# Optimization experiments

Hardware: AMD Instinct MI355X
Metric: run time of the kernel (lower is better)

## Reference

```python
import jax, jax.numpy as jnp
import numpy as np

Q, L = 512, 4096


def setup_inputs() -> dict:
    key = jax.random.key(0)
    ks = jax.random.split(key, 12)
    def rn(k, shape, s=0.05):
        return jax.random.normal(k, shape, jnp.float32) * s
    return {
        "reactions": jax.random.normal(ks[0], (1, Q, 256), jnp.float32),
        "protein":   jax.random.normal(ks[1], (1, L, 1024), jnp.float32),
        # conv1d(1024->256, k=1) == pointwise linear
        "Wc":  rn(ks[2], (256, 1024)), "bc":  jnp.zeros((256,), jnp.float32),
        "W1":  rn(ks[3], (64, 256)),   "b1":  jnp.zeros((64,), jnp.float32),
        "W2":  rn(ks[4], (64, 256)),   "b2":  jnp.zeros((64,), jnp.float32),
        "Wa":  rn(ks[5], (64, 64)),    "ba":  jnp.zeros((64,), jnp.float32),
        "Wpa": rn(ks[6], (64, 64)),    "bpa": jnp.zeros((64,), jnp.float32),
        "Wra": rn(ks[7], (64, 64)),    "bra": jnp.zeros((64,), jnp.float32),
        "Wf1": rn(ks[8], (256, 128)),  "bf1": jnp.zeros((256,), jnp.float32),
        "Wf2": rn(ks[9], (128, 256)),  "bf2": jnp.zeros((128,), jnp.float32),
        "Wf3": rn(ks[10], (1, 128)),   "bf3": jnp.zeros((1,), jnp.float32),
    }


def reference(reactions, protein, Wc, bc, W1, b1, W2, b2, Wa, ba,
              Wpa, bpa, Wra, bra, Wf1, bf1, Wf2, bf2, Wf3, bf3):
    # protein: [1, L, 1024] -> 1x1 conv over channels == linear -> [L, 256]
    p = jax.nn.relu(protein[0] @ Wc.T + bc)
    # reactions: [1, Q, 256] -> [Q, 64]
    r = jax.nn.relu(reactions[0] @ W2.T + b2)
    # protein tokens -> [L, 64]
    k = jax.nn.relu(p @ W1.T + b1)

    ra = r @ Wra.T + bra            # [Q, 64]
    pa = k @ Wpa.T + bpa            # [L, 64]
    # broadcast outer-sum + relu + small linear: [Q, L, 64]
    A = jax.nn.relu(ra[:, None, :] + pa[None, :, :]) @ Wa.T + ba

    r_gate = jax.nn.sigmoid(jnp.mean(A, axis=1))   # [Q, 64]
    p_gate = jax.nn.sigmoid(jnp.mean(A, axis=0))   # [L, 64]

    rxnfp = r + r * r_gate                          # [Q, 64]
    prot = jnp.max(k + k * p_gate, axis=0)          # [64]  maxpool over L

    ctx = jnp.concatenate(
        [rxnfp, jnp.broadcast_to(prot, (rxnfp.shape[0], 64))], axis=1)  # [Q,128]

    # dropout layers are identity in eval mode
    h = jax.nn.leaky_relu(ctx @ Wf1.T + bf1)
    h = jax.nn.leaky_relu(h @ Wf2.T + bf2)
    out = h @ Wf3.T + bf3
    return out.reshape(-1)                          # [Q]
```

## Files before the change

### kernel.cpp

```cpp
#include <hip/hip_runtime.h>
#include <hip/hip_bf16.h>
#include <math.h>

#define TPB 256

typedef __attribute__((ext_vector_type(8))) short s16x8;
typedef __attribute__((ext_vector_type(4))) float f32x4;

#define MFMA16(a, b, c) __builtin_amdgcn_mfma_f32_16x16x32_bf16((a), (b), (c), 0, 0, 0)

constexpr unsigned OFF_P    = 0u;
constexpr unsigned OFF_K    = OFF_P    + 4096u*256u;
constexpr unsigned OFF_PA   = OFF_K    + 4096u*64u;
constexpr unsigned OFF_R    = OFF_PA   + 4096u*64u;
constexpr unsigned OFF_RA   = OFF_R    + 512u*64u;
constexpr unsigned OFF_SR   = OFF_RA   + 512u*64u;
constexpr unsigned OFF_PMAX = OFF_SR   + 512u*64u;
constexpr unsigned OFF_SP   = OFF_PMAX + 64u;

__device__ __forceinline__ short f2bf(float x) {
  union { float f; unsigned u; } v; v.f = x;
  unsigned r = v.u + 0x7FFFu + ((v.u >> 16) & 1u);
  return (short)(r >> 16);
}
__device__ __forceinline__ unsigned pkbf(float a, float b) {
  __hip_bfloat162 h = __float22bfloat162_rn(make_float2(a, b));
  union { __hip_bfloat162 h2; unsigned u; } v; v.h2 = h;
  return v.u;
}
union U8 { s16x8 s; unsigned u[4]; };

__global__ __launch_bounds__(TPB, 2) void k1_gemm(
    const float* __restrict__ prot, const float* __restrict__ Wc,
    const float* __restrict__ bc,   float* __restrict__ ws)
{
  int bid = blockIdx.x;
  int tid = threadIdx.x;
  if (bid >= 512) {
    int tb = bid - 512;
    if (tb < 2) {
      unsigned base = OFF_SR + (unsigned)tb * 16384u;
#pragma unroll
      for (int it = 0; it < 16; ++it) {
        int idx = it * TPB + tid;
        *(float4*)&ws[base + (unsigned)idx * 4u] = make_float4(0.f, 0.f, 0.f, 0.f);
      }
      if (tb == 1 && tid < 16)
        *(float4*)&ws[OFF_PMAX + tid * 4] = make_float4(0.f, 0.f, 0.f, 0.f);
    } else {
      unsigned base = OFF_SP + (unsigned)(tb - 2) * 32768u;
#pragma unroll
      for (int it = 0; it < 32; ++it) {
        int idx = it * TPB + tid;
        *(float4*)&ws[base + (unsigned)idx * 4u] = make_float4(0.f, 0.f, 0.f, 0.f);
      }
    }
    return;
  }

  __shared__ __align__(16) short Asm[32 * 72];
  __shared__ __align__(16) short Bsm[64 * 72];

  int m0 = (bid >> 2) * 32;
  int n0 = (bid & 3) * 64;
  int wave = tid >> 6, lane = tid & 63;
  int wm = (wave & 1) * 16, wn = (wave >> 1) * 32;
  int lm = lane & 15, quad = lane >> 4;

  int arow = tid >> 3, aseg = (tid & 7) * 8;
  int brow = tid >> 2, bseg = (tid & 3) * 16;

  const float* Ag = prot + (size_t)(m0 + arow) * 1024 + aseg;
  const float* Bg = Wc   + (size_t)(n0 + brow) * 1024 + bseg;

  float4 a4[2], b4[4];
#pragma unroll
  for (int i = 0; i < 2; ++i) a4[i] = *(const float4*)(Ag + i * 4);
#pragma unroll
  for (int i = 0; i < 4; ++i) b4[i] = *(const float4*)(Bg + i * 4);

  f32x4 acc[2] = {};

  for (int kc = 0; kc < 16; ++kc) {
    __syncthreads();
    {
      U8 s;
      s.u[0] = pkbf(a4[0].x, a4[0].y); s.u[1] = pkbf(a4[0].z, a4[0].w);
      s.u[2] = pkbf(a4[1].x, a4[1].y); s.u[3] = pkbf(a4[1].z, a4[1].w);
      *(s16x8*)&Asm[arow * 72 + aseg] = s.s;
    }
#pragma unroll
    for (int h = 0; h < 2; ++h) {
      U8 s;
      s.u[0] = pkbf(b4[h*2].x,   b4[h*2].y);
      s.u[1] = pkbf(b4[h*2].z,   b4[h*2].w);
      s.u[2] = pkbf(b4[h*2+1].x, b4[h*2+1].y);
      s.u[3] = pkbf(b4[h*2+1].z, b4[h*2+1].w);
      *(s16x8*)&Bsm[brow * 72 + bseg + h * 8] = s.s;
    }
    if (kc < 15) {
#pragma unroll
      for (int i = 0; i < 2; ++i) a4[i] = *(const float4*)(Ag + (kc + 1) * 64 + i * 4);
#pragma unroll
      for (int i = 0; i < 4; ++i) b4[i] = *(const float4*)(Bg + (kc + 1) * 64 + i * 4);
    }
    __syncthreads();
#pragma unroll
    for (int ks = 0; ks < 2; ++ks) {
      s16x8 af = *(const s16x8*)&Asm[(wm + lm) * 72 + ks * 32 + quad * 8];
#pragma unroll
      for (int ni = 0; ni < 2; ++ni) {
        s16x8 bfv = *(const s16x8*)&Bsm[(wn + ni * 16 + lm) * 72 + ks * 32 + quad * 8];
        acc[ni] = MFMA16(af, bfv, acc[ni]);
      }
    }
  }

#pragma unroll
  for (int ni = 0; ni < 2; ++ni) {
    int col = n0 + wn + ni * 16 + lm;
    float bcv = bc[col];
#pragma unroll
    for (int r = 0; r < 4; ++r) {
      int row = m0 + wm + quad * 4 + r;
      ws[OFF_P + (unsigned)row * 256u + col] = fmaxf(acc[ni][r] + bcv, 0.f);
    }
  }
}

__global__ __launch_bounds__(TPB, 2) void k2_heads(
    const float* __restrict__ reactions,
    const float* __restrict__ W1,  const float* __restrict__ b1,
    const float* __restrict__ W2,  const float* __restrict__ b2,
    const float* __restrict__ Wpa, const float* __restrict__ bpa,
    const float* __restrict__ Wra, const float* __restrict__ bra,
    float* __restrict__ ws)
{
  __shared__ __align__(16) short Asm[32 * 264];
  __shared__ __align__(16) short Bsm[64 * 264];
  __shared__ __align__(16) short Ksm[32 * 72];
  __shared__ __align__(16) short Wsm[64 * 72];
  int bid = blockIdx.x, tid = threadIdx.x;
  bool isProt = bid < 128;
  int row0 = (isProt ? bid : (bid - 128)) * 32;
  const float* src  = isProt ? (ws + OFF_P) : reactions;
  const float* Wst1 = isProt ? W1 : W2;
  const float* bv   = isProt ? b1 : b2;
  const float* Wst2 = isProt ? Wpa : Wra;
  const float* b2nd = isProt ? bpa : bra;
  float* out1 = ws + (isProt ? OFF_K : OFF_R);
  float* out2 = ws + (isProt ? OFF_PA : OFF_RA);

  {
    int row = tid >> 3, seg = (tid & 7) * 32;
    const float* sp = src + (size_t)(row0 + row) * 256 + seg;
    float4 f[8];
#pragma unroll
    for (int i = 0; i < 8; ++i) f[i] = *(const float4*)(sp + i * 4);
#pragma unroll
    for (int i = 0; i < 4; ++i) {
      U8 s;
      s.u[0] = pkbf(f[2*i].x,   f[2*i].y);
      s.u[1] = pkbf(f[2*i].z,   f[2*i].w);
      s.u[2] = pkbf(f[2*i+1].x, f[2*i+1].y);
      s.u[3] = pkbf(f[2*i+1].z, f[2*i+1].w);
      *(s16x8*)&Asm[row * 264 + seg + i * 8] = s.s;
    }
  }
  {
    int row = tid >> 2, seg = (tid & 3) * 64;
    const float* sp = Wst1 + (size_t)row * 256 + seg;
#pragma unroll
    for (int i = 0; i < 8; ++i) {
      float4 fa = *(const float4*)(sp + i * 8);
      float4 fb = *(const float4*)(sp + i * 8 + 4);
      U8 s;
      s.u[0] = pkbf(fa.x, fa.y); s.u[1] = pkbf(fa.z, fa.w);
      s.u[2] = pkbf(fb.x, fb.y); s.u[3] = pkbf(fb.z, fb.w);
      *(s16x8*)&Bsm[row * 264 + seg + i * 8] = s.s;
    }
  }
  {
    int row = tid >> 2, seg = (tid & 3) * 16;
    const float* sp = Wst2 + (size_t)row * 64 + seg;
#pragma unroll
    for (int i = 0; i < 2; ++i) {
      float4 fa = *(const float4*)(sp + i * 8);
      float4 fb = *(const float4*)(sp + i * 8 + 4);
      U8 s;
      s.u[0] = pkbf(fa.x, fa.y); s.u[1] = pkbf(fa.z, fa.w);
      s.u[2] = pkbf(fb.x, fb.y); s.u[3] = pkbf(fb.z, fb.w);
      *(s16x8*)&Wsm[row * 72 + seg + i * 8] = s.s;
    }
  }
  __syncthreads();

  int wave = tid >> 6, lane = tid & 63;
  int lm = lane & 15, quad = lane >> 4;
  int wm = (wave >> 1) * 16, wn = (wave & 1) * 32;

  f32x4 acc[2] = {};
#pragma unroll
  for (int kc = 0; kc < 8; ++kc) {
    s16x8 a = *(const s16x8*)&Asm[(wm + lm) * 264 + kc * 32 + quad * 8];
#pragma unroll
    for (int ni = 0; ni < 2; ++ni) {
      s16x8 b = *(const s16x8*)&Bsm[(wn + ni * 16 + lm) * 264 + kc * 32 + quad * 8];
      acc[ni] = MFMA16(a, b, acc[ni]);
    }
  }
#pragma unroll
  for (int ni = 0; ni < 2; ++ni) {
    int col = wn + ni * 16 + lm;
    float bb = bv[col];
#pragma unroll
    for (int r = 0; r < 4; ++r) {
      int row = wm + quad * 4 + r;
      float kv = fmaxf(acc[ni][r] + bb, 0.f);
      out1[(size_t)(row0 + row) * 64 + col] = kv;
      Ksm[row * 72 + col] = f2bf(kv);
    }
  }
  __syncthreads();

  f32x4 acc2[2] = {};
#pragma unroll
  for (int kc = 0; kc < 2; ++kc) {
    s16x8 a = *(const s16x8*)&Ksm[(wm + lm) * 72 + kc * 32 + quad * 8];
#pragma unroll
    for (int ni = 0; ni < 2; ++ni) {
      s16x8 b = *(const s16x8*)&Wsm[(wn + ni * 16 + lm) * 72 + kc * 32 + quad * 8];
      acc2[ni] = MFMA16(a, b, acc2[ni]);
    }
  }
#pragma unroll
  for (int ni = 0; ni < 2; ++ni) {
    int col = wn + ni * 16 + lm;
    float bb = b2nd[col];
#pragma unroll
    for (int r = 0; r < 4; ++r) {
      int row = wm + quad * 4 + r;
      out2[(size_t)(row0 + row) * 64 + col] = acc2[ni][r] + bb;
    }
  }
}

__global__ __launch_bounds__(TPB, 4) void k3_interact(float* __restrict__ ws)
{
  __shared__ float sm[8192];
  int bid = blockIdx.x, tid = threadIdx.x;
  int c = tid & 63, g = tid >> 6;
  const float* ra = ws + OFF_RA;
  const float* pa = ws + OFF_PA;

  int b = bid >> 1;
  const float *X, *Y;
  unsigned x0, y0;
  float* OUT;
  if ((bid & 1) == 0) {
    x0 = (unsigned)(b >> 5) * 16;
    y0 = (unsigned)(b & 31) * 128;
    X = ra; Y = pa; OUT = ws + OFF_SR;
  } else {
    x0 = (unsigned)(b >> 2) * 16;
    y0 = (unsigned)(b & 3) * 128;
    X = pa; Y = ra; OUT = ws + OFF_SP;
  }

  int srow = tid >> 4, sc4 = (tid & 15) * 4;
  const float* src = Y + (size_t)y0 * 64;
#pragma unroll
  for (int it = 0; it < 8; ++it) {
    int row = it * 16 + srow;
    *(float4*)&sm[row * 64 + sc4] = *(const float4*)(src + row * 64 + sc4);
  }
  float u[4], acc[4];
#pragma unroll
  for (int i = 0; i < 4; ++i) {
    u[i] = X[(x0 + g * 4 + i) * 64u + c];
    acc[i] = 0.f;
  }
  __syncthreads();
#pragma unroll 8
  for (int l = 0; l < 128; ++l) {
    float x = sm[l * 64 + c];
#pragma unroll
    for (int i = 0; i < 4; ++i) acc[i] += fmaxf(u[i] + x, 0.f);
  }
#pragma unroll
  for (int i = 0; i < 4; ++i)
    atomicAdd(&OUT[(x0 + g * 4 + i) * 64u + c], acc[i]);
}

__global__ __launch_bounds__(TPB) void k3b_gate(
    const float* __restrict__ Wa, const float* __restrict__ ba,
    float* __restrict__ ws)
{
  __shared__ float sp[16 * 64];
  __shared__ float wat[64 * 65];
  int bid = blockIdx.x, tid = threadIdx.x;
  int c = tid & 63, g = tid >> 6;
  int l0 = bid * 16;
  {
    int idx = tid * 4;
    float4 v = *(const float4*)&ws[OFF_SP + (unsigned)l0 * 64u + idx];
    v.x *= (1.f / 512.f); v.y *= (1.f / 512.f);
    v.z *= (1.f / 512.f); v.w *= (1.f / 512.f);
    *(float4*)&sp[idx] = v;
  }
  for (int it = 0; it < 16; ++it) {
    int idx = it * TPB + tid;
    wat[(idx & 63) * 65 + (idx >> 6)] = Wa[idx];
  }
  __syncthreads();
  float vmax = 0.f;
  float bac = ba[c];
#pragma unroll
  for (int i = 0; i < 4; ++i) {
    int ll = g * 4 + i;
    float dot = 0.f;
#pragma unroll 8
    for (int jj = 0; jj < 64; ++jj)
      dot += sp[ll * 64 + jj] * wat[jj * 65 + c];
    float pg = 1.f / (1.f + __expf(-(dot + bac)));
    float val = ws[OFF_K + (unsigned)(l0 + ll) * 64u + c] * (1.f + pg);
    vmax = fmaxf(vmax, val);
  }
  atomicMax((int*)&ws[OFF_PMAX + c], __float_as_int(vmax));
}

__global__ __launch_bounds__(TPB) void k4_final(
    const float* __restrict__ Wa,  const float* __restrict__ ba,
    const float* __restrict__ Wf1, const float* __restrict__ bf1,
    const float* __restrict__ Wf2, const float* __restrict__ bf2,
    const float* __restrict__ Wf3, const float* __restrict__ bf3,
    float* __restrict__ ws, float* __restrict__ out)
{
  __shared__ __align__(16) short mrb[16 * 72];
  __shared__ __align__(16) short wab[64 * 72];
  __shared__ __align__(16) short ctxb[16 * 136];
  __shared__ __align__(16) short h1b[16 * 264];
  __shared__ __align__(16) short wgt[256 * 136];
  __shared__ float red[64];
  int bid = blockIdx.x, tid = threadIdx.x;
  int q0 = bid * 16;
  int wave = tid >> 6, lane = tid & 63;
  int lm = lane & 15, quad = lane >> 4;

  {
    int q = tid >> 4, c4 = (tid & 15) * 4;
    float4 v = *(const float4*)&ws[OFF_SR + (unsigned)(q0 + q) * 64u + c4];
    uint2 st = make_uint2(pkbf(v.x * (1.f/4096.f), v.y * (1.f/4096.f)),
                          pkbf(v.z * (1.f/4096.f), v.w * (1.f/4096.f)));
    *(uint2*)&mrb[q * 72 + c4] = st;
  }
#pragma unroll
  for (int it = 0; it < 4; ++it) {
    int i4 = it * TPB + tid;
    int row = i4 >> 4, c4 = (i4 & 15) * 4;
    float4 v = *(const float4*)&Wa[row * 64 + c4];
    uint2 st = make_uint2(pkbf(v.x, v.y), pkbf(v.z, v.w));
    *(uint2*)&wab[row * 72 + c4] = st;
  }
  __syncthreads();

  f32x4 gacc = {};
#pragma unroll
  for (int kc = 0; kc < 2; ++kc) {
    s16x8 a = *(const s16x8*)&mrb[lm * 72 + kc * 32 + quad * 8];
    s16x8 b = *(const s16x8*)&wab[(wave * 16 + lm) * 72 + kc * 32 + quad * 8];
    gacc = MFMA16(a, b, gacc);
  }
  {
    int c = wave * 16 + lm;
    float bac = ba[c];
    short pb = f2bf(ws[OFF_PMAX + c]);
#pragma unroll
    for (int r = 0; r < 4; ++r) {
      int q = quad * 4 + r;
      float gg = 1.f / (1.f + __expf(-(gacc[r] + bac)));
      float rv = ws[OFF_R + (unsigned)(q0 + q) * 64u + c];
      ctxb[q * 136 + c]      = f2bf(rv * (1.f + gg));
      ctxb[q * 136 + 64 + c] = pb;
    }
  }
#pragma unroll 4
  for (int it = 0; it < 32; ++it) {
    int i4 = it * TPB + tid;
    int row = i4 >> 5, c4 = (i4 & 31) * 4;
    float4 v = *(const float4*)&Wf1[row * 128 + c4];
    uint2 st = make_uint2(pkbf(v.x, v.y), pkbf(v.z, v.w));
    *(uint2*)&wgt[row * 136 + c4] = st;
  }
  __syncthreads();

  f32x4 h[4] = {};
#pragma unroll
  for (int kc = 0; kc < 4; ++kc) {
    s16x8 a = *(const s16x8*)&ctxb[lm * 136 + kc * 32 + quad * 8];
#pragma unroll
    for (int nt = 0; nt < 4; ++nt) {
      s16x8 b = *(const s16x8*)&wgt[(wave * 64 + nt * 16 + lm) * 136 + kc * 32 + quad * 8];
      h[nt] = MFMA16(a, b, h[nt]);
    }
  }
#pragma unroll
  for (int nt = 0; nt < 4; ++nt) {
    int n = wave * 64 + nt * 16 + lm;
    float bb = bf1[n];
#pragma unroll
    for (int r = 0; r < 4; ++r) {
      int q = quad * 4 + r;
      float v = h[nt][r] + bb;
      v = v > 0.f ? v : 0.01f * v;
      h1b[q * 264 + n] = f2bf(v);
    }
  }
  __syncthreads();

#pragma unroll 4
  for (int it = 0; it < 32; ++it) {
    int i4 = it * TPB + tid;
    int row = i4 >> 6, c4 = (i4 & 63) * 4;
    float4 v = *(const float4*)&Wf2[row * 256 + c4];
    uint2 st = make_uint2(pkbf(v.x, v.y), pkbf(v.z, v.w));
    *(uint2*)&wgt[row * 264 + c4] = st;
  }
  __syncthreads();

  f32x4 o[2] = {};
#pragma unroll
  for (int kc = 0; kc < 8; ++kc) {
    s16x8 a = *(const s16x8*)&h1b[lm * 264 + kc * 32 + quad * 8];
#pragma unroll
    for (int nt = 0; nt < 2; ++nt) {
      s16x8 b = *(const s16x8*)&wgt[(wave * 32 + nt * 16 + lm) * 264 + kc * 32 + quad * 8];
      o[nt] = MFMA16(a, b, o[nt]);
    }
  }
  float pv[4] = {0.f, 0.f, 0.f, 0.f};
#pragma unroll
  for (int nt = 0; nt < 2; ++nt) {
    int m = wave * 32 + nt * 16 + lm;
    float bb = bf2[m], w3 = Wf3[m];
#pragma unroll
    for (int r = 0; r < 4; ++r) {
      float v = o[nt][r] + bb;
      v = v > 0.f ? v : 0.01f * v;
      pv[r] += v * w3;
    }
  }
#pragma unroll
  for (int msk = 1; msk < 16; msk <<= 1)
#pragma unroll
    for (int r = 0; r < 4; ++r) pv[r] += __shfl_xor(pv[r], msk);
  if (lm == 0) {
#pragma unroll
    for (int r = 0; r < 4; ++r) red[(quad * 4 + r) * 4 + wave] = pv[r];
  }
  __syncthreads();
  if (tid < 16)
    out[q0 + tid] = red[tid * 4] + red[tid * 4 + 1] + red[tid * 4 + 2] +
                    red[tid * 4 + 3] + bf3[0];
}

extern "C" void kernel_launch(void* const* d_in, const int* in_sizes, int n_in,
                              void* d_out, int out_size, void* d_ws, size_t ws_size,
                              hipStream_t stream)
{
  const float* reactions = (const float*)d_in[0];
  const float* protein   = (const float*)d_in[1];
  const float* Wc  = (const float*)d_in[2];
  const float* bc  = (const float*)d_in[3];
  const float* W1  = (const float*)d_in[4];
  const float* b1  = (const float*)d_in[5];
  const float* W2  = (const float*)d_in[6];
  const float* b2  = (const float*)d_in[7];
  const float* Wa  = (const float*)d_in[8];
  const float* ba  = (const float*)d_in[9];
  const float* Wpa = (const float*)d_in[10];
  const float* bpa = (const float*)d_in[11];
  const float* Wra = (const float*)d_in[12];
  const float* bra = (const float*)d_in[13];
  const float* Wf1 = (const float*)d_in[14];
  const float* bf1 = (const float*)d_in[15];
  const float* Wf2 = (const float*)d_in[16];
  const float* bf2 = (const float*)d_in[17];
  const float* Wf3 = (const float*)d_in[18];
  const float* bf3 = (const float*)d_in[19];
  float* ws  = (float*)d_ws;
  float* out = (float*)d_out;

  hipLaunchKernelGGL(k1_gemm, dim3(522), dim3(TPB), 0, stream,
                     protein, Wc, bc, ws);
  hipLaunchKernelGGL(k2_heads, dim3(144), dim3(TPB), 0, stream,
                     reactions, W1, b1, W2, b2, Wpa, bpa, Wra, bra, ws);
  hipLaunchKernelGGL(k3_interact, dim3(2048), dim3(TPB), 0, stream, ws);
  hipLaunchKernelGGL(k3b_gate, dim3(256), dim3(TPB), 0, stream, Wa, ba, ws);
  hipLaunchKernelGGL(k4_final, dim3(32), dim3(TPB), 0, stream,
                     Wa, ba, Wf1, bf1, Wf2, bf2, Wf3, bf3, ws, out);
}
```

Before: 174.4 us.

## Replace atomic accumulation with partial-sum buffers reduced in consumer kernels

The interaction kernel now writes per-tile partial sums into separate slices (32 slices for the reaction means, 4 for the protein means) with plain stores instead of atomicAdd into one buffer. The gate and final kernels sum these partials as they load them, and the k1 zeroing blocks are dropped except for the pmax clear. This removes atomic contention and the zero-init pass, at the cost of a larger workspace and extra reads in the consumers (32 loads per element in k4, which runs on only 32 blocks).

```diff
diff --git a/kernel.cpp b/kernel.cpp
--- a/kernel.cpp
+++ b/kernel.cpp
@@ -14,9 +14,9 @@
 constexpr unsigned OFF_PA   = OFF_K    + 4096u*64u;
 constexpr unsigned OFF_R    = OFF_PA   + 4096u*64u;
 constexpr unsigned OFF_RA   = OFF_R    + 512u*64u;
-constexpr unsigned OFF_SR   = OFF_RA   + 512u*64u;
-constexpr unsigned OFF_PMAX = OFF_SR   + 512u*64u;
-constexpr unsigned OFF_SP   = OFF_PMAX + 64u;
+constexpr unsigned OFF_PMAX = OFF_RA   + 512u*64u;
+constexpr unsigned OFF_SRP  = OFF_PMAX + 64u;
+constexpr unsigned OFF_SPP  = OFF_SRP  + 32u*512u*64u;
 
 __device__ __forceinline__ short f2bf(float x) {
   union { float f; unsigned u; } v; v.f = x;
@@ -37,24 +37,8 @@
   int bid = blockIdx.x;
   int tid = threadIdx.x;
   if (bid >= 512) {
-    int tb = bid - 512;
-    if (tb < 2) {
-      unsigned base = OFF_SR + (unsigned)tb * 16384u;
-#pragma unroll
-      for (int it = 0; it < 16; ++it) {
-        int idx = it * TPB + tid;
-        *(float4*)&ws[base + (unsigned)idx * 4u] = make_float4(0.f, 0.f, 0.f, 0.f);
-      }
-      if (tb == 1 && tid < 16)
-        *(float4*)&ws[OFF_PMAX + tid * 4] = make_float4(0.f, 0.f, 0.f, 0.f);
-    } else {
-      unsigned base = OFF_SP + (unsigned)(tb - 2) * 32768u;
-#pragma unroll
-      for (int it = 0; it < 32; ++it) {
-        int idx = it * TPB + tid;
-        *(float4*)&ws[base + (unsigned)idx * 4u] = make_float4(0.f, 0.f, 0.f, 0.f);
-      }
-    }
+    if (tid < 16)
+      *(float4*)&ws[OFF_PMAX + tid * 4] = make_float4(0.f, 0.f, 0.f, 0.f);
     return;
   }
 
@@ -260,11 +244,13 @@
   if ((bid & 1) == 0) {
     x0 = (unsigned)(b >> 5) * 16;
     y0 = (unsigned)(b & 31) * 128;
-    X = ra; Y = pa; OUT = ws + OFF_SR;
+    X = ra; Y = pa;
+    OUT = ws + OFF_SRP + (unsigned)(b & 31) * (512u * 64u);
   } else {
     x0 = (unsigned)(b >> 2) * 16;
     y0 = (unsigned)(b & 3) * 128;
-    X = pa; Y = ra; OUT = ws + OFF_SP;
+    X = pa; Y = ra;
+    OUT = ws + OFF_SPP + (unsigned)(b & 3) * (4096u * 64u);
   }
 
   int srow = tid >> 4, sc4 = (tid & 15) * 4;
@@ -289,7 +275,7 @@
   }
 #pragma unroll
   for (int i = 0; i < 4; ++i)
-    atomicAdd(&OUT[(x0 + g * 4 + i) * 64u + c], acc[i]);
+    OUT[(x0 + g * 4 + i) * 64u + c] = acc[i];
 }
 
 __global__ __launch_bounds__(TPB) void k3b_gate(
@@ -302,11 +288,16 @@
   int c = tid & 63, g = tid >> 6;
   int l0 = bid * 16;
   {
-    int idx = tid * 4;
-    float4 v = *(const float4*)&ws[OFF_SP + (unsigned)l0 * 64u + idx];
-    v.x *= (1.f / 512.f); v.y *= (1.f / 512.f);
-    v.z *= (1.f / 512.f); v.w *= (1.f / 512.f);
-    *(float4*)&sp[idx] = v;
+    unsigned idx = (unsigned)l0 * 64u + tid * 4;
+    float4 s = make_float4(0.f, 0.f, 0.f, 0.f);
+#pragma unroll
+    for (int p = 0; p < 4; ++p) {
+      float4 v = *(const float4*)&ws[OFF_SPP + (unsigned)p * (4096u * 64u) + idx];
+      s.x += v.x; s.y += v.y; s.z += v.z; s.w += v.w;
+    }
+    s.x *= (1.f / 512.f); s.y *= (1.f / 512.f);
+    s.z *= (1.f / 512.f); s.w *= (1.f / 512.f);
+    *(float4*)&sp[tid * 4] = s;
   }
   for (int it = 0; it < 16; ++it) {
     int idx = it * TPB + tid;
@@ -349,9 +340,15 @@
 
   {
     int q = tid >> 4, c4 = (tid & 15) * 4;
-    float4 v = *(const float4*)&ws[OFF_SR + (unsigned)(q0 + q) * 64u + c4];
-    uint2 st = make_uint2(pkbf(v.x * (1.f/4096.f), v.y * (1.f/4096.f)),
-                          pkbf(v.z * (1.f/4096.f), v.w * (1.f/4096.f)));
+    unsigned idx = (unsigned)(q0 + q) * 64u + c4;
+    float4 s = make_float4(0.f, 0.f, 0.f, 0.f);
+#pragma unroll 8
+    for (int p = 0; p < 32; ++p) {
+      float4 v = *(const float4*)&ws[OFF_SRP + (unsigned)p * (512u * 64u) + idx];
+      s.x += v.x; s.y += v.y; s.z += v.z; s.w += v.w;
+    }
+    uint2 st = make_uint2(pkbf(s.x * (1.f/4096.f), s.y * (1.f/4096.f)),
+                          pkbf(s.z * (1.f/4096.f), s.w * (1.f/4096.f)));
     *(uint2*)&mrb[q * 72 + c4] = st;
   }
 #pragma unroll
@@ -491,7 +488,7 @@
   float* ws  = (float*)d_ws;
   float* out = (float*)d_out;
 
-  hipLaunchKernelGGL(k1_gemm, dim3(522), dim3(TPB), 0, stream,
+  hipLaunchKernelGGL(k1_gemm, dim3(513), dim3(TPB), 0, stream,
                      protein, Wc, bc, ws);
   hipLaunchKernelGGL(k2_heads, dim3(144), dim3(TPB), 0, stream,
                      reactions, W1, b1, W2, b2, Wpa, bpa, Wra, bra, ws);
```

Result: no change. 176.7 us (+1.3%).

## Replace pairwise relu-sum interaction with per-channel histogram prefix sums

Applied to the files above, without the earlier changes.

The pairwise O(Q·L·64) accumulation of relu(ra+pa) is replaced by a per-channel method. Each channel bins the protein values, or the reaction values, into a 1024-bin histogram of counts and sums, then takes suffix prefix sums. Each query is then answered as u·count(x>-u) + sum(x>-u) by a bin lookup, so the atomic accumulation and the workspace zeroing are no longer needed. The result is approximate within one bin width around the threshold. The work now runs on only 64 blocks, and the column gathers into shared memory are strided.

```diff
diff --git a/kernel.cpp b/kernel.cpp
--- a/kernel.cpp
+++ b/kernel.cpp
@@ -37,24 +37,8 @@
   int bid = blockIdx.x;
   int tid = threadIdx.x;
   if (bid >= 512) {
-    int tb = bid - 512;
-    if (tb < 2) {
-      unsigned base = OFF_SR + (unsigned)tb * 16384u;
-#pragma unroll
-      for (int it = 0; it < 16; ++it) {
-        int idx = it * TPB + tid;
-        *(float4*)&ws[base + (unsigned)idx * 4u] = make_float4(0.f, 0.f, 0.f, 0.f);
-      }
-      if (tb == 1 && tid < 16)
-        *(float4*)&ws[OFF_PMAX + tid * 4] = make_float4(0.f, 0.f, 0.f, 0.f);
-    } else {
-      unsigned base = OFF_SP + (unsigned)(tb - 2) * 32768u;
-#pragma unroll
-      for (int it = 0; it < 32; ++it) {
-        int idx = it * TPB + tid;
-        *(float4*)&ws[base + (unsigned)idx * 4u] = make_float4(0.f, 0.f, 0.f, 0.f);
-      }
-    }
+    if (tid < 16)
+      *(float4*)&ws[OFF_PMAX + tid * 4] = make_float4(0.f, 0.f, 0.f, 0.f);
     return;
   }
 
@@ -245,51 +229,135 @@
   }
 }
 
-__global__ __launch_bounds__(TPB, 4) void k3_interact(float* __restrict__ ws)
+__global__ __launch_bounds__(TPB) void k3h_hist(float* __restrict__ ws)
 {
-  __shared__ float sm[8192];
-  int bid = blockIdx.x, tid = threadIdx.x;
-  int c = tid & 63, g = tid >> 6;
+  __shared__ float xcol[4096];
+  __shared__ float rcol[512];
+  __shared__ float hc[1025];
+  __shared__ float hs[1025];
+  __shared__ float rmn[4], rmx[4];
+  int c = blockIdx.x, tid = threadIdx.x;
+  int wave = tid >> 6, lane = tid & 63;
+  const float* pa = ws + OFF_PA;
   const float* ra = ws + OFF_RA;
-  const float* pa = ws + OFF_PA;
-
-  int b = bid >> 1;
-  const float *X, *Y;
-  unsigned x0, y0;
-  float* OUT;
-  if ((bid & 1) == 0) {
-    x0 = (unsigned)(b >> 5) * 16;
-    y0 = (unsigned)(b & 31) * 128;
-    X = ra; Y = pa; OUT = ws + OFF_SR;
-  } else {
-    x0 = (unsigned)(b >> 2) * 16;
-    y0 = (unsigned)(b & 3) * 128;
-    X = pa; Y = ra; OUT = ws + OFF_SP;
-  }
-
-  int srow = tid >> 4, sc4 = (tid & 15) * 4;
-  const float* src = Y + (size_t)y0 * 64;
-#pragma unroll
-  for (int it = 0; it < 8; ++it) {
-    int row = it * 16 + srow;
-    *(float4*)&sm[row * 64 + sc4] = *(const float4*)(src + row * 64 + sc4);
-  }
-  float u[4], acc[4];
-#pragma unroll
-  for (int i = 0; i < 4; ++i) {
-    u[i] = X[(x0 + g * 4 + i) * 64u + c];
-    acc[i] = 0.f;
-  }
-  __syncthreads();
-#pragma unroll 8
-  for (int l = 0; l < 128; ++l) {
-    float x = sm[l * 64 + c];
-#pragma unroll
-    for (int i = 0; i < 4; ++i) acc[i] += fmaxf(u[i] + x, 0.f);
-  }
-#pragma unroll
-  for (int i = 0; i < 4; ++i)
-    atomicAdd(&OUT[(x0 + g * 4 + i) * 64u + c], acc[i]);
+
+  for (int i = tid; i < 4096; i += TPB) xcol[i] = pa[(unsigned)i * 64u + c];
+  for (int i = tid; i < 512;  i += TPB) rcol[i] = ra[(unsigned)i * 64u + c];
+  for (int i = tid; i < 1025; i += TPB) { hc[i] = 0.f; hs[i] = 0.f; }
+  __syncthreads();
+
+  float mn = 1e30f, mx = -1e30f;
+  for (int i = tid; i < 4096; i += TPB) {
+    float x = xcol[i];
+    mn = fminf(mn, x); mx = fmaxf(mx, x);
+  }
+#pragma unroll
+  for (int off = 32; off > 0; off >>= 1) {
+    mn = fminf(mn, __shfl_down(mn, off));
+    mx = fmaxf(mx, __shfl_down(mx, off));
+  }
+  if (lane == 0) { rmn[wave] = mn; rmx[wave] = mx; }
+  __syncthreads();
+  mn = fminf(fminf(rmn[0], rmn[1]), fminf(rmn[2], rmn[3]));
+  mx = fmaxf(fmaxf(rmx[0], rmx[1]), fmaxf(rmx[2], rmx[3]));
+  float w = (mx - mn) * (1.f / 1024.f);
+  float invw = (w > 1e-30f) ? 1.f / w : 0.f;
+  for (int i = tid; i < 4096; i += TPB) {
+    float x = xcol[i];
+    int b = (int)((x - mn) * invw);
+    b = b < 0 ? 0 : (b > 1023 ? 1023 : b);
+    atomicAdd(&hc[b], 1.f);
+    atomicAdd(&hs[b], x);
+  }
+  __syncthreads();
+  if (wave == 0) {
+    float vc[16], vs[16], sc = 0.f, ss = 0.f;
+#pragma unroll
+    for (int i = 0; i < 16; ++i) {
+      vc[i] = hc[lane * 16 + i]; sc += vc[i];
+      vs[i] = hs[lane * 16 + i]; ss += vs[i];
+    }
+    float tc = sc, ts = ss;
+#pragma unroll
+    for (int off = 1; off < 64; off <<= 1) {
+      float oc = __shfl_down(tc, off);
+      float os = __shfl_down(ts, off);
+      if (lane + off < 64) { tc += oc; ts += os; }
+    }
+    float runc = tc - sc, runs = ts - ss;
+#pragma unroll
+    for (int i = 15; i >= 0; --i) {
+      runc += vc[i]; hc[lane * 16 + i] = runc;
+      runs += vs[i]; hs[lane * 16 + i] = runs;
+    }
+  }
+  __syncthreads();
+  for (int q = tid; q < 512; q += TPB) {
+    float u = rcol[q];
+    float thr = -u;
+    int b;
+    if (thr < mn) b = 0;
+    else { b = (int)((thr - mn) * invw) + 1; b = b > 1024 ? 1024 : b; }
+    ws[OFF_SR + (unsigned)q * 64u + c] = u * hc[b] + hs[b];
+  }
+  __syncthreads();
+
+  for (int i = tid; i < 1025; i += TPB) { hc[i] = 0.f; hs[i] = 0.f; }
+  float mn2 = 1e30f, mx2 = -1e30f;
+  for (int i = tid; i < 512; i += TPB) {
+    float x = rcol[i];
+    mn2 = fminf(mn2, x); mx2 = fmaxf(mx2, x);
+  }
+#pragma unroll
+  for (int off = 32; off > 0; off >>= 1) {
+    mn2 = fminf(mn2, __shfl_down(mn2, off));
+    mx2 = fmaxf(mx2, __shfl_down(mx2, off));
+  }
+  __syncthreads();
+  if (lane == 0) { rmn[wave] = mn2; rmx[wave] = mx2; }
+  __syncthreads();
+  mn2 = fminf(fminf(rmn[0], rmn[1]), fminf(rmn[2], rmn[3]));
+  mx2 = fmaxf(fmaxf(rmx[0], rmx[1]), fmaxf(rmx[2], rmx[3]));
+  float w2 = (mx2 - mn2) * (1.f / 1024.f);
+  float invw2 = (w2 > 1e-30f) ? 1.f / w2 : 0.f;
+  for (int i = tid; i < 512; i += TPB) {
+    float x = rcol[i];
+    int b = (int)((x - mn2) * invw2);
+    b = b < 0 ? 0 : (b > 1023 ? 1023 : b);
+    atomicAdd(&hc[b], 1.f);
+    atomicAdd(&hs[b], x);
+  }
+  __syncthreads();
+  if (wave == 0) {
+    float vc[16], vs[16], sc = 0.f, ss = 0.f;
+#pragma unroll
+    for (int i = 0; i < 16; ++i) {
+      vc[i] = hc[lane * 16 + i]; sc += vc[i];
+      vs[i] = hs[lane * 16 + i]; ss += vs[i];
+    }
+    float tc = sc, ts = ss;
+#pragma unroll
+    for (int off = 1; off < 64; off <<= 1) {
+      float oc = __shfl_down(tc, off);
+      float os = __shfl_down(ts, off);
+      if (lane + off < 64) { tc += oc; ts += os; }
+    }
+    float runc = tc - sc, runs = ts - ss;
+#pragma unroll
+    for (int i = 15; i >= 0; --i) {
+      runc += vc[i]; hc[lane * 16 + i] = runc;
+      runs += vs[i]; hs[lane * 16 + i] = runs;
+    }
+  }
+  __syncthreads();
+  for (int l = tid; l < 4096; l += TPB) {
+    float v = xcol[l];
+    float thr = -v;
+    int b;
+    if (thr < mn2) b = 0;
+    else { b = (int)((thr - mn2) * invw2) + 1; b = b > 1024 ? 1024 : b; }
+    ws[OFF_SP + (unsigned)l * 64u + c] = v * hc[b] + hs[b];
+  }
 }
 
 __global__ __launch_bounds__(TPB) void k3b_gate(
@@ -491,11 +559,11 @@
   float* ws  = (float*)d_ws;
   float* out = (float*)d_out;
 
-  hipLaunchKernelGGL(k1_gemm, dim3(522), dim3(TPB), 0, stream,
+  hipLaunchKernelGGL(k1_gemm, dim3(513), dim3(TPB), 0, stream,
                      protein, Wc, bc, ws);
   hipLaunchKernelGGL(k2_heads, dim3(144), dim3(TPB), 0, stream,
                      reactions, W1, b1, W2, b2, Wpa, bpa, Wra, bra, ws);
-  hipLaunchKernelGGL(k3_interact, dim3(2048), dim3(TPB), 0, stream, ws);
+  hipLaunchKernelGGL(k3h_hist, dim3(64), dim3(TPB), 0, stream, ws);
   hipLaunchKernelGGL(k3b_gate, dim3(256), dim3(TPB), 0, stream, Wa, ba, ws);
   hipLaunchKernelGGL(k4_final, dim3(32), dim3(TPB), 0, stream,
                      Wa, ba, Wf1, bf1, Wf2, bf2, Wf3, bf3, ws, out);
```

Measured after the change: 178.5 us. 2.3% more time.
